# Kernel tuning notes

Hardware: AMD Instinct MI355X
Metric: run time of the kernel (lower is better)

## Reference

```python
import jax, jax.numpy as jnp
import numpy as np

N_USER = 50000
N_ITEM = 100000
N = N_USER + N_ITEM
D = 64
NNZ = 2_400_000
B = 4096
N_LAYERS = 3
NEG_SLOPE = 0.01  # F.leaky_relu default
EPS = 1e-12       # F.normalize default eps


def setup_inputs() -> dict:
    key = jax.random.key(0)
    ks = jax.random.split(key, 12)
    s = 0.1  # xavier-ish scale
    return {
        "user_emb": jax.random.normal(ks[0], (N_USER, D), jnp.float32) * s,
        "item_emb": jax.random.normal(ks[1], (N_ITEM, D), jnp.float32) * s,
        "W_gc": jax.random.normal(ks[2], (N_LAYERS, D, D), jnp.float32) * s,
        "W_bi": jax.random.normal(ks[3], (N_LAYERS, D, D), jnp.float32) * s,
        "b_bi": jax.random.normal(ks[4], (N_LAYERS, 1, D), jnp.float32) * s,
        "vals": jax.random.uniform(ks[5], (NNZ,), jnp.float32) * (1.0 / 16.0),
        "rows": jax.random.randint(ks[6], (NNZ,), 0, N, jnp.int32),
        "cols": jax.random.randint(ks[7], (NNZ,), 0, N, jnp.int32),
        "users": jax.random.randint(ks[8], (B,), 0, N_USER, jnp.int32),
        "pos_items": jax.random.randint(ks[9], (B,), 0, N_ITEM, jnp.int32),
        "neg_items": jax.random.randint(ks[10], (B,), 0, N_ITEM, jnp.int32),
    }


def _spmm(rows, cols, vals, E, n):
    # sparse [n,n] (COO) @ dense [n,d]
    return jax.ops.segment_sum(vals[:, None] * E[cols], rows, num_segments=n)


def reference(user_emb, item_emb, W_gc, W_bi, b_bi, vals, rows, cols,
              users, pos_items, neg_items):
    n_user = user_emb.shape[0]
    n = n_user + item_emb.shape[0]
    ego = jnp.concatenate([user_emb, item_emb], axis=0)  # [N, D]
    all_embs = [ego]
    for k in range(N_LAYERS):
        L_side = _spmm(rows, cols, vals, ego, n)        # L @ E
        LI_side = L_side + ego                           # (L + I) @ E
        # NOTE: original code adds b_bi to BOTH branches (b_gc unused)
        sum_e = LI_side @ W_gc[k] + b_bi[k]
        bi_e = (L_side * ego) @ W_bi[k] + b_bi[k]
        ego = jax.nn.leaky_relu(sum_e + bi_e, NEG_SLOPE)
        norm = ego / jnp.maximum(
            jnp.linalg.norm(ego, axis=1, keepdims=True), EPS)
        all_embs.append(norm)
    all_embs = jnp.concatenate(all_embs, axis=1)         # [N, D*(L+1)]
    u_g = all_embs[:n_user][users]
    pos_g = all_embs[n_user:][pos_items]
    neg_g = all_embs[n_user:][neg_items]
    return (u_g, pos_g, neg_g)
```

## Files before the change

### kernel.cpp

```cpp
#include <hip/hip_runtime.h>

#define N_USER 50000
#define N_ITEM 100000
#define NTOT   150000
#define D      64
#define NNZ    2400000
#define NEG_SLOPE 0.01f

#define BSHIFT 10
#define NB     147
#define P1_PER 4096
#define NBLK1  586

typedef unsigned int uint;
typedef unsigned short ushort;

__device__ inline uint bf16rne(float x) {
    uint b = __float_as_uint(x);
    return (b + 0x7FFFu + ((b >> 16) & 1u)) >> 16;
}
__device__ inline float bf_lo(uint u) { return __uint_as_float(u << 16); }
__device__ inline float bf_hi(uint u) { return __uint_as_float(u & 0xFFFF0000u); }

__global__ void k_concat16(const float* __restrict__ u, const float* __restrict__ it,
                           ushort* __restrict__ A16) {
    int i = blockIdx.x * 256 + threadIdx.x;
    const int nu4 = N_USER * D / 4;
    float4 v = (i < nu4) ? ((const float4*)u)[i] : ((const float4*)it)[i - nu4];
    uint lo = bf16rne(v.x) | (bf16rne(v.y) << 16);
    uint hi = bf16rne(v.z) | (bf16rne(v.w) << 16);
    ((uint2*)A16)[i] = make_uint2(lo, hi);
}

__global__ void k_bzero(int* __restrict__ bcnt) {
    int t = threadIdx.x;
    if (t < NB) bcnt[t] = 0;
}

__global__ __launch_bounds__(1024) void k_bhist(const int* __restrict__ rows,
                                                int* __restrict__ bcnt) {
    __shared__ int lcnt[NB];
    int tid = threadIdx.x;
    if (tid < NB) lcnt[tid] = 0;
    __syncthreads();
    int base = blockIdx.x * P1_PER;
    #pragma unroll
    for (int k = 0; k < 4; ++k) {
        int i = base + k * 1024 + tid;
        if (i < NNZ) atomicAdd(&lcnt[rows[i] >> BSHIFT], 1);
    }
    __syncthreads();
    if (tid < NB) atomicAdd(&bcnt[tid], lcnt[tid]);
}

__global__ void k_bscan(const int* __restrict__ bcnt, int* __restrict__ bptr,
                        int* __restrict__ bcur) {
    __shared__ int s[256];
    int tid = threadIdx.x;
    int v = (tid < NB) ? bcnt[tid] : 0;
    s[tid] = v; __syncthreads();
    for (int off = 1; off < 256; off <<= 1) {
        int t = (tid >= off) ? s[tid - off] : 0;
        __syncthreads();
        s[tid] += t;
        __syncthreads();
    }
    if (tid < NB) { int ex = s[tid] - v; bptr[tid] = ex; bcur[tid] = ex; }
    if (tid == NB - 1) bptr[NB] = s[tid];
}

__global__ __launch_bounds__(1024) void k_binpass1(const int* __restrict__ rows,
                                                   const int* __restrict__ cols,
                                                   const float* __restrict__ vals,
                                                   int* __restrict__ bcur,
                                                   int2* __restrict__ bucketed) {
    __shared__ int lcnt[NB], lbase[NB];
    int tid = threadIdx.x;
    int base = blockIdx.x * P1_PER;
    if (tid < NB) lcnt[tid] = 0;
    __syncthreads();
    int r[4];
    #pragma unroll
    for (int k = 0; k < 4; ++k) {
        int i = base + k * 1024 + tid;
        r[k] = (i < NNZ) ? rows[i] : -1;
        if (r[k] >= 0) atomicAdd(&lcnt[r[k] >> BSHIFT], 1);
    }
    __syncthreads();
    if (tid < NB) { lbase[tid] = atomicAdd(&bcur[tid], lcnt[tid]); lcnt[tid] = 0; }
    __syncthreads();
    #pragma unroll
    for (int k = 0; k < 4; ++k) {
        int i = base + k * 1024 + tid;
        if (r[k] >= 0) {
            int b = r[k] >> BSHIFT;
            int off = atomicAdd(&lcnt[b], 1);
            bucketed[lbase[b] + off] =
                make_int2(((r[k] & 1023) << 18) | cols[i], __float_as_int(vals[i]));
        }
    }
}

__global__ __launch_bounds__(1024) void k_binpass2(const int* __restrict__ bptr,
                                                   const int2* __restrict__ bucketed,
                                                   int* __restrict__ ptr,
                                                   int2* __restrict__ csr) {
    __shared__ int c0[1024], px[1024];
    int tid = threadIdx.x, b = blockIdx.x;
    int s = bptr[b], e = bptr[b + 1];
    c0[tid] = 0;
    __syncthreads();
    for (int i = s + tid; i < e; i += 1024) atomicAdd(&c0[bucketed[i].x >> 18], 1);
    __syncthreads();
    int v = c0[tid];
    px[tid] = v;
    __syncthreads();
    for (int off = 1; off < 1024; off <<= 1) {
        int t = (tid >= off) ? px[tid - off] : 0;
        __syncthreads();
        px[tid] += t;
        __syncthreads();
    }
    int ex = px[tid] - v;
    int r = (b << BSHIFT) + tid;
    if (r <= NTOT) ptr[r] = s + ex;
    px[tid] = ex;
    c0[tid] = 0;
    __syncthreads();
    for (int i = s + tid; i < e; i += 1024) {
        int2 e2 = bucketed[i];
        int lr = e2.x >> 18;
        int off = atomicAdd(&c0[lr], 1);
        csr[s + px[lr] + off] = make_int2(e2.x & 0x3FFFF, e2.y);
    }
}

__global__ __launch_bounds__(256) void k_spmm(const int* __restrict__ ptr,
                                              const int2* __restrict__ csr,
                                              const ushort* __restrict__ E16,
                                              float* __restrict__ Lout) {
    int lane = threadIdx.x & 63;
    int half = lane >> 5;
    int l32  = lane & 31;
    int r = __builtin_amdgcn_readfirstlane(blockIdx.x * 4 + (threadIdx.x >> 6));
    int start = ptr[r], end = ptr[r + 1];
    float acc0 = 0.f, acc1 = 0.f;
    const uint* E32 = (const uint*)E16;
    int j = start;
    for (; j + 7 < end; j += 8) {
        int2 ea = csr[j + 0], eb = csr[j + 1];
        int2 ec = csr[j + 2], ed = csr[j + 3];
        int2 ee = csr[j + 4], ef = csr[j + 5];
        int2 eg = csr[j + 6], eh = csr[j + 7];
        int c0 = half ? eb.x : ea.x;
        int c1 = half ? ed.x : ec.x;
        int c2 = half ? ef.x : ee.x;
        int c3 = half ? eh.x : eg.x;
        uint u0 = E32[(c0 << 5) + l32];
        uint u1 = E32[(c1 << 5) + l32];
        uint u2 = E32[(c2 << 5) + l32];
        uint u3 = E32[(c3 << 5) + l32];
        float v0 = __int_as_float(half ? eb.y : ea.y);
        float v1 = __int_as_float(half ? ed.y : ec.y);
        float v2 = __int_as_float(half ? ef.y : ee.y);
        float v3 = __int_as_float(half ? eh.y : eg.y);
        acc0 += v0 * bf_lo(u0);  acc1 += v0 * bf_hi(u0);
        acc0 += v1 * bf_lo(u1);  acc1 += v1 * bf_hi(u1);
        acc0 += v2 * bf_lo(u2);  acc1 += v2 * bf_hi(u2);
        acc0 += v3 * bf_lo(u3);  acc1 += v3 * bf_hi(u3);
    }
    for (; j + 1 < end; j += 2) {
        int2 ea = csr[j], eb = csr[j + 1];
        int c   = half ? eb.x : ea.x;
        float v = __int_as_float(half ? eb.y : ea.y);
        uint u = E32[(c << 5) + l32];
        acc0 += v * bf_lo(u);  acc1 += v * bf_hi(u);
    }
    if (j < end) {
        int2 ea = csr[j];
        if (half == 0) {
            uint u = E32[(ea.x << 5) + l32];
            float v = __int_as_float(ea.y);
            acc0 += v * bf_lo(u);  acc1 += v * bf_hi(u);
        }
    }
    acc0 += __shfl_xor(acc0, 32, 64);
    acc1 += __shfl_xor(acc1, 32, 64);
    if (half == 0)
        *(float2*)&Lout[r * D + l32 * 2] = make_float2(acc0, acc1);
}

__global__ __launch_bounds__(256) void k_transform(const ushort* __restrict__ E16,
                                                   const float* __restrict__ L,
                                                   const float* __restrict__ Wgc,
                                                   const float* __restrict__ Wbi,
                                                   const float* __restrict__ bb,
                                                   ushort* __restrict__ O16, int n) {
    __shared__ float xT[2 * D][D];
    __shared__ float W2[2 * D][D];
    int tid = threadIdx.x;
    int rowbase = blockIdx.x * 64;

    for (int i = tid; i < 128 * 16; i += 256) {
        int k = i >> 4, q = i & 15;
        const float* src = (k < D) ? (Wgc + k * D + q * 4) : (Wbi + (k - D) * D + q * 4);
        *(float4*)&W2[k][q * 4] = *(const float4*)src;
    }
    {
        int row = tid >> 2;
        int cg  = (tid & 3) * 16;
        int r   = rowbase + row;
        for (int j = 0; j < 4; ++j) {
            int c = cg + j * 4;
            float4 l = make_float4(0, 0, 0, 0);
            uint2  eu = make_uint2(0, 0);
            if (r < n) {
                l  = *(const float4*)&L[r * D + c];
                eu = *(const uint2*)&E16[r * D + c];
            }
            float e0 = bf_lo(eu.x), e1 = bf_hi(eu.x), e2 = bf_lo(eu.y), e3 = bf_hi(eu.y);
            xT[c + 0][row] = l.x + e0;  xT[D + c + 0][row] = l.x * e0;
            xT[c + 1][row] = l.y + e1;  xT[D + c + 1][row] = l.y * e1;
            xT[c + 2][row] = l.z + e2;  xT[D + c + 2][row] = l.z * e2;
            xT[c + 3][row] = l.w + e3;  xT[D + c + 3][row] = l.w * e3;
        }
    }
    __syncthreads();

    int tx = tid & 15, ty = tid >> 4;
    float acc[4][4];
    #pragma unroll
    for (int i = 0; i < 4; ++i)
        #pragma unroll
        for (int j = 0; j < 4; ++j) acc[i][j] = 0.f;

    #pragma unroll 4
    for (int k = 0; k < 2 * D; ++k) {
        float4 a = *(const float4*)&xT[k][ty * 4];
        float4 b = *(const float4*)&W2[k][tx * 4];
        float av[4] = {a.x, a.y, a.z, a.w};
        float bv[4] = {b.x, b.y, b.z, b.w};
        #pragma unroll
        for (int i = 0; i < 4; ++i)
            #pragma unroll
            for (int j = 0; j < 4; ++j) acc[i][j] += av[i] * bv[j];
    }

    float4 bias = *(const float4*)&bb[tx * 4];
    float bv[4] = {bias.x, bias.y, bias.z, bias.w};
    #pragma unroll
    for (int i = 0; i < 4; ++i) {
        int r = rowbase + ty * 4 + i;
        if (r < n) {
            float o[4];
            #pragma unroll
            for (int j = 0; j < 4; ++j) {
                float y = acc[i][j] + 2.f * bv[j];
                o[j] = (y >= 0.f) ? y : NEG_SLOPE * y;
            }
            uint lo = bf16rne(o[0]) | (bf16rne(o[1]) << 16);
            uint hi = bf16rne(o[2]) | (bf16rne(o[3]) << 16);
            *(uint2*)&O16[r * D + tx * 4] = make_uint2(lo, hi);
        }
    }
}

__global__ void k_gather0(const float* __restrict__ u, const float* __restrict__ it,
                          const int* __restrict__ users, const int* __restrict__ pos,
                          const int* __restrict__ neg, float* __restrict__ out) {
    int lane = threadIdx.x & 63;
    int gi = blockIdx.x * 4 + (threadIdx.x >> 6);
    int g = gi >> 12, b = gi & 4095;
    const float* src = (g == 0) ? (u + (size_t)users[b] * D)
                                : (it + (size_t)((g == 1) ? pos[b] : neg[b]) * D);
    out[gi * 256 + lane] = src[lane];
}

__global__ void k_gathern(const ushort* __restrict__ E16, const int* __restrict__ users,
                          const int* __restrict__ pos, const int* __restrict__ neg,
                          float* __restrict__ out, int layer) {
    int lane = threadIdx.x & 63;
    int gi = blockIdx.x * 4 + (threadIdx.x >> 6);
    int g = gi >> 12, b = gi & 4095;
    int src = (g == 0) ? users[b] : (N_USER + ((g == 1) ? pos[b] : neg[b]));
    float v = __uint_as_float(((uint)E16[src * D + lane]) << 16);
    float ss = v * v;
    #pragma unroll
    for (int off = 32; off >= 1; off >>= 1) ss += __shfl_xor(ss, off, 64);
    float dnm = fmaxf(sqrtf(ss), 1e-12f);
    out[gi * 256 + layer * D + lane] = v / dnm;
}

extern "C" void kernel_launch(void* const* d_in, const int* in_sizes, int n_in,
                              void* d_out, int out_size, void* d_ws, size_t ws_size,
                              hipStream_t stream) {
    const float* user_emb = (const float*)d_in[0];
    const float* item_emb = (const float*)d_in[1];
    const float* W_gc     = (const float*)d_in[2];
    const float* W_bi     = (const float*)d_in[3];
    const float* b_bi     = (const float*)d_in[4];
    const float* vals     = (const float*)d_in[5];
    const int*   rows     = (const int*)d_in[6];
    const int*   cols     = (const int*)d_in[7];
    const int*   users    = (const int*)d_in[8];
    const int*   pos      = (const int*)d_in[9];
    const int*   neg      = (const int*)d_in[10];
    float* out = (float*)d_out;

    char* ws = (char*)d_ws;
    size_t off = 0;
    auto alloc = [&](size_t b) { void* p = ws + off; off += (b + 255) & ~(size_t)255; return p; };
    ushort* Ea  = (ushort*)alloc((size_t)NTOT * D * 2);
    ushort* Eb  = (ushort*)alloc((size_t)NTOT * D * 2);
    float*  L   = (float*) alloc((size_t)NTOT * D * 4);
    int2*   csr = (int2*)  alloc((size_t)NNZ * 8);
    int*    ptr = (int*)   alloc((size_t)(NTOT + 1) * 4);
    int*    bptr= (int*)   alloc((NB + 1) * 4);
    int*    bcnt= (int*)   alloc(NB * 4);
    int*    bcur= (int*)   alloc(NB * 4);
    int2*   bucketed = (int2*)L;
    (void)ws_size;

    hipLaunchKernelGGL(k_concat16, dim3(9375), dim3(256),  0, stream, user_emb, item_emb, Ea);
    hipLaunchKernelGGL(k_bzero,    dim3(1),    dim3(256),  0, stream, bcnt);
    hipLaunchKernelGGL(k_bhist,    dim3(NBLK1),dim3(1024), 0, stream, rows, bcnt);
    hipLaunchKernelGGL(k_bscan,    dim3(1),    dim3(256),  0, stream, bcnt, bptr, bcur);
    hipLaunchKernelGGL(k_binpass1, dim3(NBLK1),dim3(1024), 0, stream, rows, cols, vals, bcur, bucketed);
    hipLaunchKernelGGL(k_binpass2, dim3(NB),   dim3(1024), 0, stream, bptr, bucketed, ptr, csr);
    hipLaunchKernelGGL(k_gather0,  dim3(3072), dim3(256),  0, stream, user_emb, item_emb, users, pos, neg, out);

    ushort* cur = Ea; ushort* nxt = Eb;
    for (int k = 0; k < 3; ++k) {
        hipLaunchKernelGGL(k_spmm,      dim3(37500), dim3(256), 0, stream, ptr, csr, cur, L);
        hipLaunchKernelGGL(k_transform, dim3(2344),  dim3(256), 0, stream, cur, L,
                           W_gc + k * 4096, W_bi + k * 4096, b_bi + k * 64, nxt, NTOT);
        hipLaunchKernelGGL(k_gathern,   dim3(3072),  dim3(256), 0, stream, nxt, users, pos, neg, out, k + 1);
        ushort* t = cur; cur = nxt; nxt = t;
    }
}
```

Measured before the change: 543.0 us.

## Use MFMA fp16 for layer transform and deepen SpMM gather unroll

Replaces the scalar FP32 LDS-tiled GEMM in the per-layer transform with MFMA 16x16x16 fp16 matrix instructions. Weights are converted to fp16 fragments once per block, and each block processes four 64-row tiles, staging output through LDS for coalesced bf16 stores. The SpMM main loop is also unrolled to 16 edges so more gathers are in flight per iteration. This lowers ALU and LDS cost in the transform, but inputs are rounded to fp16, which risks precision loss, and the larger unroll raises register use.

```diff
diff --git a/kernel.cpp b/kernel.cpp
--- a/kernel.cpp
+++ b/kernel.cpp
@@ -14,6 +14,8 @@
 
 typedef unsigned int uint;
 typedef unsigned short ushort;
+typedef _Float16 h4 __attribute__((ext_vector_type(4)));
+typedef float f4 __attribute__((ext_vector_type(4)));
 
 __device__ inline uint bf16rne(float x) {
     uint b = __float_as_uint(x);
@@ -147,27 +149,37 @@
     float acc0 = 0.f, acc1 = 0.f;
     const uint* E32 = (const uint*)E16;
     int j = start;
+    for (; j + 15 < end; j += 16) {
+        int2 q[16];
+        #pragma unroll
+        for (int i = 0; i < 16; ++i) q[i] = csr[j + i];
+        uint u[8]; float v[8];
+        #pragma unroll
+        for (int i = 0; i < 8; ++i) {
+            int c = half ? q[2 * i + 1].x : q[2 * i].x;
+            v[i] = __int_as_float(half ? q[2 * i + 1].y : q[2 * i].y);
+            u[i] = E32[(c << 5) + l32];
+        }
+        #pragma unroll
+        for (int i = 0; i < 8; ++i) {
+            acc0 += v[i] * bf_lo(u[i]);  acc1 += v[i] * bf_hi(u[i]);
+        }
+    }
     for (; j + 7 < end; j += 8) {
-        int2 ea = csr[j + 0], eb = csr[j + 1];
-        int2 ec = csr[j + 2], ed = csr[j + 3];
-        int2 ee = csr[j + 4], ef = csr[j + 5];
-        int2 eg = csr[j + 6], eh = csr[j + 7];
-        int c0 = half ? eb.x : ea.x;
-        int c1 = half ? ed.x : ec.x;
-        int c2 = half ? ef.x : ee.x;
-        int c3 = half ? eh.x : eg.x;
-        uint u0 = E32[(c0 << 5) + l32];
-        uint u1 = E32[(c1 << 5) + l32];
-        uint u2 = E32[(c2 << 5) + l32];
-        uint u3 = E32[(c3 << 5) + l32];
-        float v0 = __int_as_float(half ? eb.y : ea.y);
-        float v1 = __int_as_float(half ? ed.y : ec.y);
-        float v2 = __int_as_float(half ? ef.y : ee.y);
-        float v3 = __int_as_float(half ? eh.y : eg.y);
-        acc0 += v0 * bf_lo(u0);  acc1 += v0 * bf_hi(u0);
-        acc0 += v1 * bf_lo(u1);  acc1 += v1 * bf_hi(u1);
-        acc0 += v2 * bf_lo(u2);  acc1 += v2 * bf_hi(u2);
-        acc0 += v3 * bf_lo(u3);  acc1 += v3 * bf_hi(u3);
+        int2 q[8];
+        #pragma unroll
+        for (int i = 0; i < 8; ++i) q[i] = csr[j + i];
+        uint u[4]; float v[4];
+        #pragma unroll
+        for (int i = 0; i < 4; ++i) {
+            int c = half ? q[2 * i + 1].x : q[2 * i].x;
+            v[i] = __int_as_float(half ? q[2 * i + 1].y : q[2 * i].y);
+            u[i] = E32[(c << 5) + l32];
+        }
+        #pragma unroll
+        for (int i = 0; i < 4; ++i) {
+            acc0 += v[i] * bf_lo(u[i]);  acc1 += v[i] * bf_hi(u[i]);
+        }
     }
     for (; j + 1 < end; j += 2) {
         int2 ea = csr[j], eb = csr[j + 1];
@@ -190,77 +202,93 @@
         *(float2*)&Lout[r * D + l32 * 2] = make_float2(acc0, acc1);
 }
 
-__global__ __launch_bounds__(256) void k_transform(const ushort* __restrict__ E16,
-                                                   const float* __restrict__ L,
-                                                   const float* __restrict__ Wgc,
-                                                   const float* __restrict__ Wbi,
-                                                   const float* __restrict__ bb,
-                                                   ushort* __restrict__ O16, int n) {
-    __shared__ float xT[2 * D][D];
-    __shared__ float W2[2 * D][D];
+__global__ __launch_bounds__(256) void k_transform_mfma(
+        const ushort* __restrict__ E16, const float* __restrict__ L,
+        const float* __restrict__ Wgc, const float* __restrict__ Wbi,
+        const float* __restrict__ bb, ushort* __restrict__ O16, int n) {
+    __shared__ _Float16 ldsW[2 * 16 * 256];
+    __shared__ ushort   ldsO[4][16 * 72];
     int tid = threadIdx.x;
-    int rowbase = blockIdx.x * 64;
-
-    for (int i = tid; i < 128 * 16; i += 256) {
-        int k = i >> 4, q = i & 15;
-        const float* src = (k < D) ? (Wgc + k * D + q * 4) : (Wbi + (k - D) * D + q * 4);
-        *(float4*)&W2[k][q * 4] = *(const float4*)src;
-    }
-    {
-        int row = tid >> 2;
-        int cg  = (tid & 3) * 16;
-        int r   = rowbase + row;
-        for (int j = 0; j < 4; ++j) {
-            int c = cg + j * 4;
-            float4 l = make_float4(0, 0, 0, 0);
-            uint2  eu = make_uint2(0, 0);
-            if (r < n) {
-                l  = *(const float4*)&L[r * D + c];
-                eu = *(const uint2*)&E16[r * D + c];
+
+    #pragma unroll
+    for (int m = 0; m < 2; ++m) {
+        const float* W = m ? Wbi : Wgc;
+        for (int idx = tid; idx < 4096; idx += 256) {
+            int k = idx >> 6, nn = idx & 63;
+            ldsW[(m * 16 + (k >> 4) * 4 + (nn >> 4)) * 256 + (nn & 15) * 16 + (k & 15)] =
+                (_Float16)W[idx];
+        }
+    }
+    __syncthreads();
+
+    int l = tid & 63, w = tid >> 6;
+    int g = l >> 4, r16 = l & 15;
+
+    h4 bfrag[2][4][4];
+    #pragma unroll
+    for (int m = 0; m < 2; ++m)
+        #pragma unroll
+        for (int ks = 0; ks < 4; ++ks)
+            #pragma unroll
+            for (int nt = 0; nt < 4; ++nt)
+                bfrag[m][ks][nt] =
+                    *(const h4*)&ldsW[(m * 16 + ks * 4 + nt) * 256 + r16 * 16 + g * 4];
+
+    for (int t = 0; t < 4; ++t) {
+        int tile = blockIdx.x * 4 + t;
+        int rowbase = tile * 64 + w * 16;
+        int r = rowbase + r16;
+        int rc = min(r, n - 1);
+
+        h4 x1[4], x2[4];
+        #pragma unroll
+        for (int ks = 0; ks < 4; ++ks) {
+            int c = ks * 16 + g * 4;
+            float4 lf = *(const float4*)&L[rc * D + c];
+            uint2  eu = *(const uint2*)&E16[rc * D + c];
+            float e0 = bf_lo(eu.x), e1 = bf_hi(eu.x);
+            float e2 = bf_lo(eu.y), e3 = bf_hi(eu.y);
+            x1[ks][0] = (_Float16)(lf.x + e0); x1[ks][1] = (_Float16)(lf.y + e1);
+            x1[ks][2] = (_Float16)(lf.z + e2); x1[ks][3] = (_Float16)(lf.w + e3);
+            x2[ks][0] = (_Float16)(lf.x * e0); x2[ks][1] = (_Float16)(lf.y * e1);
+            x2[ks][2] = (_Float16)(lf.z * e2); x2[ks][3] = (_Float16)(lf.w * e3);
+        }
+
+        f4 acc[4];
+        #pragma unroll
+        for (int nt = 0; nt < 4; ++nt) acc[nt] = (f4){0.f, 0.f, 0.f, 0.f};
+        #pragma unroll
+        for (int ks = 0; ks < 4; ++ks)
+            #pragma unroll
+            for (int nt = 0; nt < 4; ++nt)
+                acc[nt] = __builtin_amdgcn_mfma_f32_16x16x16f16(x1[ks], bfrag[0][ks][nt],
+                                                                acc[nt], 0, 0, 0);
+        #pragma unroll
+        for (int ks = 0; ks < 4; ++ks)
+            #pragma unroll
+            for (int nt = 0; nt < 4; ++nt)
+                acc[nt] = __builtin_amdgcn_mfma_f32_16x16x16f16(x2[ks], bfrag[1][ks][nt],
+                                                                acc[nt], 0, 0, 0);
+
+        #pragma unroll
+        for (int nt = 0; nt < 4; ++nt) {
+            int col = nt * 16 + r16;
+            float bv = 2.f * bb[col];
+            #pragma unroll
+            for (int i = 0; i < 4; ++i) {
+                float y = acc[nt][i] + bv;
+                y = (y >= 0.f) ? y : NEG_SLOPE * y;
+                ldsO[w][(g * 4 + i) * 72 + col] = (ushort)bf16rne(y);
             }
-            float e0 = bf_lo(eu.x), e1 = bf_hi(eu.x), e2 = bf_lo(eu.y), e3 = bf_hi(eu.y);
-            xT[c + 0][row] = l.x + e0;  xT[D + c + 0][row] = l.x * e0;
-            xT[c + 1][row] = l.y + e1;  xT[D + c + 1][row] = l.y * e1;
-            xT[c + 2][row] = l.z + e2;  xT[D + c + 2][row] = l.z * e2;
-            xT[c + 3][row] = l.w + e3;  xT[D + c + 3][row] = l.w * e3;
-        }
-    }
-    __syncthreads();
-
-    int tx = tid & 15, ty = tid >> 4;
-    float acc[4][4];
-    #pragma unroll
-    for (int i = 0; i < 4; ++i)
-        #pragma unroll
-        for (int j = 0; j < 4; ++j) acc[i][j] = 0.f;
-
-    #pragma unroll 4
-    for (int k = 0; k < 2 * D; ++k) {
-        float4 a = *(const float4*)&xT[k][ty * 4];
-        float4 b = *(const float4*)&W2[k][tx * 4];
-        float av[4] = {a.x, a.y, a.z, a.w};
-        float bv[4] = {b.x, b.y, b.z, b.w};
-        #pragma unroll
-        for (int i = 0; i < 4; ++i)
-            #pragma unroll
-            for (int j = 0; j < 4; ++j) acc[i][j] += av[i] * bv[j];
-    }
-
-    float4 bias = *(const float4*)&bb[tx * 4];
-    float bv[4] = {bias.x, bias.y, bias.z, bias.w};
-    #pragma unroll
-    for (int i = 0; i < 4; ++i) {
-        int r = rowbase + ty * 4 + i;
-        if (r < n) {
-            float o[4];
-            #pragma unroll
-            for (int j = 0; j < 4; ++j) {
-                float y = acc[i][j] + 2.f * bv[j];
-                o[j] = (y >= 0.f) ? y : NEG_SLOPE * y;
-            }
-            uint lo = bf16rne(o[0]) | (bf16rne(o[1]) << 16);
-            uint hi = bf16rne(o[2]) | (bf16rne(o[3]) << 16);
-            *(uint2*)&O16[r * D + tx * 4] = make_uint2(lo, hi);
+        }
+        int lr = l >> 2;
+        int rowg = rowbase + lr;
+        if (rowg < n) {
+            const ushort* src = &ldsO[w][lr * 72 + (l & 3) * 16];
+            uint4 v0 = *(const uint4*)src;
+            uint4 v1 = *(const uint4*)(src + 8);
+            *(uint4*)&O16[rowg * D + (l & 3) * 16] = v0;
+            *(uint4*)&O16[rowg * D + (l & 3) * 16 + 8] = v1;
         }
     }
 }
@@ -331,10 +359,10 @@
 
     ushort* cur = Ea; ushort* nxt = Eb;
     for (int k = 0; k < 3; ++k) {
-        hipLaunchKernelGGL(k_spmm,      dim3(37500), dim3(256), 0, stream, ptr, csr, cur, L);
-        hipLaunchKernelGGL(k_transform, dim3(2344),  dim3(256), 0, stream, cur, L,
+        hipLaunchKernelGGL(k_spmm,           dim3(37500), dim3(256), 0, stream, ptr, csr, cur, L);
+        hipLaunchKernelGGL(k_transform_mfma, dim3(586),   dim3(256), 0, stream, cur, L,
                            W_gc + k * 4096, W_bi + k * 4096, b_bi + k * 64, nxt, NTOT);
-        hipLaunchKernelGGL(k_gathern,   dim3(3072),  dim3(256), 0, stream, nxt, users, pos, neg, out, k + 1);
+        hipLaunchKernelGGL(k_gathern,        dim3(3072),  dim3(256), 0, stream, nxt, users, pos, neg, out, k + 1);
         ushort* t = cur; cur = nxt; nxt = t;
     }
 }
```

Measured after the change: 794.2 us. 46.3% more time.
